# Kernel tuning notes

Hardware: AMD Instinct MI355X
Metric: run time of the kernel (lower is better)

Reference implementation:

```python
import jax, jax.numpy as jnp
import numpy as np


def setup_inputs() -> dict:
    key = jax.random.key(0)
    k1, k2, k3 = jax.random.split(key, 3)
    B, D, F = 1000000, 16, 8
    out = jax.random.normal(k1, (B, D), dtype=jnp.float32)
    target = jax.random.normal(k2, (B, D), dtype=jnp.float32)
    x = jax.random.uniform(k3, (B, F), dtype=jnp.float32)
    return {"out": out, "target": target, "x": x}


def reference(out, target, x):
    # per-sample L1 loss (mean over features), weighted by (1 + 0.1*speed),
    # then mean over the batch. speed = x[:, 3].
    per_sample_l1 = jnp.mean(jnp.abs(out - target), axis=1)  # [B]
    weight = 1.0 + x[:, 3] * 0.1                              # [B]
    return jnp.mean(per_sample_l1 * weight)                   # scalar
```

## Files before the change

### kernel.cpp

```cpp
#include <hip/hip_runtime.h>
#include <hip/hip_bf16.h>


__global__ void weighted_l1_stage1(const float4* __restrict__ outp,
                                   const float4* __restrict__ tgtp,
                                   const float* __restrict__ x,
                                   float* __restrict__ partial,
                                   int B, float inv_scale) {
    int i = blockIdx.x * blockDim.x + threadIdx.x;
    float acc = 0.0f;
    if (i < B) {
        const float4* o4 = outp + (size_t)i * 4;
        const float4* t4 = tgtp + (size_t)i * 4;
        float4 a0 = o4[0], a1 = o4[1], a2 = o4[2], a3 = o4[3];
        float4 b0 = t4[0], b1 = t4[1], b2 = t4[2], b3 = t4[3];
        float xv = x[(size_t)i * 8 + 3];

        float s = fabsf(a0.x - b0.x) + fabsf(a0.y - b0.y)
                + fabsf(a0.z - b0.z) + fabsf(a0.w - b0.w)
                + fabsf(a1.x - b1.x) + fabsf(a1.y - b1.y)
                + fabsf(a1.z - b1.z) + fabsf(a1.w - b1.w)
                + fabsf(a2.x - b2.x) + fabsf(a2.y - b2.y)
                + fabsf(a2.z - b2.z) + fabsf(a2.w - b2.w)
                + fabsf(a3.x - b3.x) + fabsf(a3.y - b3.y)
                + fabsf(a3.z - b3.z) + fabsf(a3.w - b3.w);
        float w = fmaf(0.1f, xv, 1.0f);
        acc = s * w * inv_scale;
    }

    #pragma unroll
    for (int off = 32; off > 0; off >>= 1)
        acc += __shfl_down(acc, off);

    __shared__ float wsum[4];
    int lane = threadIdx.x & 63;
    int wid  = threadIdx.x >> 6;
    if (lane == 0) wsum[wid] = acc;
    __syncthreads();
    if (threadIdx.x == 0)
        partial[blockIdx.x] = wsum[0] + wsum[1] + wsum[2] + wsum[3];
}

__global__ void weighted_l1_stage2(const float* __restrict__ partial,
                                   float* __restrict__ res, int n) {
    float acc = 0.0f;
    for (int j = threadIdx.x; j < n; j += 256)
        acc += partial[j];

    #pragma unroll
    for (int off = 32; off > 0; off >>= 1)
        acc += __shfl_down(acc, off);

    __shared__ float wsum[4];
    int lane = threadIdx.x & 63;
    int wid  = threadIdx.x >> 6;
    if (lane == 0) wsum[wid] = acc;
    __syncthreads();
    if (threadIdx.x == 0)
        res[0] = wsum[0] + wsum[1] + wsum[2] + wsum[3];
}

extern "C" void kernel_launch(void* const* d_in, const int* in_sizes, int n_in,
                              void* d_out, int out_size, void* d_ws, size_t ws_size,
                              hipStream_t stream) {
    const float* outp = (const float*)d_in[0];
    const float* tgtp = (const float*)d_in[1];
    const float* x    = (const float*)d_in[2];
    float* res = (float*)d_out;
    float* partial = (float*)d_ws;

    int B = in_sizes[0] / 16;
    int block = 256;
    int grid  = (B + block - 1) / block;

    weighted_l1_stage1<<<grid, block, 0, stream>>>(
        (const float4*)outp, (const float4*)tgtp, x, partial,
        B, 1.0f / (16.0f * (float)B));
    weighted_l1_stage2<<<1, block, 0, stream>>>(partial, res, grid);
}
```

Measured before the change: 33.41 us.

## Coalesce float4 loads across threads and process eight chunks per thread

Remaps the stage-1 reduction so consecutive threads read consecutive float4 chunks instead of each thread reading a whole 64-byte row, and each thread handles eight strided chunks with a fast full-block path and a guarded tail path. The intent is better coalescing and more loads in flight per thread, with fewer blocks and partials for the final reduction. The weight value is loaded redundantly by the four threads sharing a row, and per-row accumulation order changes slightly.

```diff
diff --git a/kernel.cpp b/kernel.cpp
--- a/kernel.cpp
+++ b/kernel.cpp
@@ -2,30 +2,58 @@
 #include <hip/hip_bf16.h>
 
 
-__global__ void weighted_l1_stage1(const float4* __restrict__ outp,
-                                   const float4* __restrict__ tgtp,
-                                   const float* __restrict__ x,
-                                   float* __restrict__ partial,
-                                   int B, float inv_scale) {
-    int i = blockIdx.x * blockDim.x + threadIdx.x;
+__global__ __launch_bounds__(256)
+void weighted_l1_stage1(const float4* __restrict__ outp,
+                        const float4* __restrict__ tgtp,
+                        const float* __restrict__ x,
+                        float* __restrict__ partial,
+                        size_t n4, float inv_scale) {
+    const int ITER = 8;
+    size_t base = (size_t)blockIdx.x * (256 * ITER) + threadIdx.x;
     float acc = 0.0f;
-    if (i < B) {
-        const float4* o4 = outp + (size_t)i * 4;
-        const float4* t4 = tgtp + (size_t)i * 4;
-        float4 a0 = o4[0], a1 = o4[1], a2 = o4[2], a3 = o4[3];
-        float4 b0 = t4[0], b1 = t4[1], b2 = t4[2], b3 = t4[3];
-        float xv = x[(size_t)i * 8 + 3];
 
-        float s = fabsf(a0.x - b0.x) + fabsf(a0.y - b0.y)
-                + fabsf(a0.z - b0.z) + fabsf(a0.w - b0.w)
-                + fabsf(a1.x - b1.x) + fabsf(a1.y - b1.y)
-                + fabsf(a1.z - b1.z) + fabsf(a1.w - b1.w)
-                + fabsf(a2.x - b2.x) + fabsf(a2.y - b2.y)
-                + fabsf(a2.z - b2.z) + fabsf(a2.w - b2.w)
-                + fabsf(a3.x - b3.x) + fabsf(a3.y - b3.y)
-                + fabsf(a3.z - b3.z) + fabsf(a3.w - b3.w);
-        float w = fmaf(0.1f, xv, 1.0f);
-        acc = s * w * inv_scale;
+    if ((size_t)(blockIdx.x + 1) * (256 * ITER) <= n4) {
+        float4 a0 = outp[base + 0 * 256], a1 = outp[base + 1 * 256],
+               a2 = outp[base + 2 * 256], a3 = outp[base + 3 * 256],
+               a4 = outp[base + 4 * 256], a5 = outp[base + 5 * 256],
+               a6 = outp[base + 6 * 256], a7 = outp[base + 7 * 256];
+        float4 b0 = tgtp[base + 0 * 256], b1 = tgtp[base + 1 * 256],
+               b2 = tgtp[base + 2 * 256], b3 = tgtp[base + 3 * 256],
+               b4 = tgtp[base + 4 * 256], b5 = tgtp[base + 5 * 256],
+               b6 = tgtp[base + 6 * 256], b7 = tgtp[base + 7 * 256];
+        float w0 = x[((base + 0 * 256) >> 2) * 8 + 3],
+              w1 = x[((base + 1 * 256) >> 2) * 8 + 3],
+              w2 = x[((base + 2 * 256) >> 2) * 8 + 3],
+              w3 = x[((base + 3 * 256) >> 2) * 8 + 3],
+              w4 = x[((base + 4 * 256) >> 2) * 8 + 3],
+              w5 = x[((base + 5 * 256) >> 2) * 8 + 3],
+              w6 = x[((base + 6 * 256) >> 2) * 8 + 3],
+              w7 = x[((base + 7 * 256) >> 2) * 8 + 3];
+
+        float s0 = fabsf(a0.x-b0.x)+fabsf(a0.y-b0.y)+fabsf(a0.z-b0.z)+fabsf(a0.w-b0.w);
+        float s1 = fabsf(a1.x-b1.x)+fabsf(a1.y-b1.y)+fabsf(a1.z-b1.z)+fabsf(a1.w-b1.w);
+        float s2 = fabsf(a2.x-b2.x)+fabsf(a2.y-b2.y)+fabsf(a2.z-b2.z)+fabsf(a2.w-b2.w);
+        float s3 = fabsf(a3.x-b3.x)+fabsf(a3.y-b3.y)+fabsf(a3.z-b3.z)+fabsf(a3.w-b3.w);
+        float s4 = fabsf(a4.x-b4.x)+fabsf(a4.y-b4.y)+fabsf(a4.z-b4.z)+fabsf(a4.w-b4.w);
+        float s5 = fabsf(a5.x-b5.x)+fabsf(a5.y-b5.y)+fabsf(a5.z-b5.z)+fabsf(a5.w-b5.w);
+        float s6 = fabsf(a6.x-b6.x)+fabsf(a6.y-b6.y)+fabsf(a6.z-b6.z)+fabsf(a6.w-b6.w);
+        float s7 = fabsf(a7.x-b7.x)+fabsf(a7.y-b7.y)+fabsf(a7.z-b7.z)+fabsf(a7.w-b7.w);
+
+        acc = s0 * fmaf(0.1f, w0, 1.0f) + s1 * fmaf(0.1f, w1, 1.0f)
+            + s2 * fmaf(0.1f, w2, 1.0f) + s3 * fmaf(0.1f, w3, 1.0f)
+            + s4 * fmaf(0.1f, w4, 1.0f) + s5 * fmaf(0.1f, w5, 1.0f)
+            + s6 * fmaf(0.1f, w6, 1.0f) + s7 * fmaf(0.1f, w7, 1.0f);
+        acc *= inv_scale;
+    } else {
+        for (int k = 0; k < ITER; ++k) {
+            size_t c = base + (size_t)k * 256;
+            if (c < n4) {
+                float4 a = outp[c], b = tgtp[c];
+                float s = fabsf(a.x-b.x)+fabsf(a.y-b.y)+fabsf(a.z-b.z)+fabsf(a.w-b.w);
+                float w = fmaf(0.1f, x[(c >> 2) * 8 + 3], 1.0f);
+                acc += s * w * inv_scale;
+            }
+        }
     }
 
     #pragma unroll
@@ -70,11 +98,15 @@
     float* partial = (float*)d_ws;
 
     int B = in_sizes[0] / 16;
+    size_t n4 = (size_t)B * 4;
+
     int block = 256;
-    int grid  = (B + block - 1) / block;
+    int chunks_per_block = block * 8;
+    int grid = (int)((n4 + chunks_per_block - 1) / chunks_per_block);
+    if (grid < 1) grid = 1;
 
     weighted_l1_stage1<<<grid, block, 0, stream>>>(
         (const float4*)outp, (const float4*)tgtp, x, partial,
-        B, 1.0f / (16.0f * (float)B));
-    weighted_l1_stage2<<<1, block, 0, stream>>>(partial, res, grid);
+        n4, 1.0f / (16.0f * (float)B));
+    weighted_l1_stage2<<<1, 256, 0, stream>>>(partial, res, grid);
 }
```

Measured after the change: 30.93 us. -7.4%, faster.
